# Kernel optimization log

Hardware: AMD Instinct MI355X
Metric: run time of the kernel (lower is better)

The kernel has to match this reference:

```python
import jax, jax.numpy as jnp
import numpy as np

LN_EPS = 1e-5

def setup_inputs() -> dict:
    key = jax.random.key(0)
    k1, k2, k3 = jax.random.split(key, 3)
    B, S, D = 4, 4096, 768
    seq_feat = jax.random.normal(k1, (B, S, D), dtype=jnp.float32)
    msa_feat = jax.random.normal(k2, (B, S, D), dtype=jnp.float32)
    ln_gamma = jnp.ones((2 * D,), dtype=jnp.float32)
    ln_beta = jnp.zeros((2 * D,), dtype=jnp.float32)
    # torch init zeroes gate weight; use small random weights for a non-degenerate test
    gate_w = jax.random.normal(k3, (2, 2 * D), dtype=jnp.float32) * 0.02
    gate_b = jnp.zeros((2,), dtype=jnp.float32)
    return {"seq_feat": seq_feat, "msa_feat": msa_feat, "ln_gamma": ln_gamma,
            "ln_beta": ln_beta, "gate_w": gate_w, "gate_b": gate_b}

def reference(seq_feat, msa_feat, ln_gamma, ln_beta, gate_w, gate_b):
    # h: [B, S, 2D]
    h = jnp.concatenate([seq_feat, msa_feat], axis=-1)
    mean = jnp.mean(h, axis=-1, keepdims=True)
    var = jnp.mean(jnp.square(h - mean), axis=-1, keepdims=True)
    hn = (h - mean) * jax.lax.rsqrt(var + LN_EPS) * ln_gamma + ln_beta
    # dropout in eval mode = identity
    logits = jnp.einsum('bsd,kd->bsk', hn, gate_w) + gate_b  # [B, S, 2]
    w = jax.nn.softmax(logits, axis=-1)
    return w[..., 0:1] * seq_feat + w[..., 1:2] * msa_feat
```

## Files before the change

### kernel.cpp

```cpp
#include <hip/hip_runtime.h>

#define LN_EPS 1e-5f
#define D 768
#define TWO_D 1536

__global__ __launch_bounds__(256) void fused_gate_kernel(
    const float* __restrict__ seq, const float* __restrict__ msa,
    const float* __restrict__ gamma, const float* __restrict__ beta,
    const float* __restrict__ gate_w, const float* __restrict__ gate_b,
    float* __restrict__ out, int nrows)
{
    const int wave = threadIdx.x >> 6;
    const int lane = threadIdx.x & 63;
    const int row = blockIdx.x * 4 + wave;
    if (row >= nrows) return;

    const float4* seq4 = (const float4*)(seq + (size_t)row * D);
    const float4* msa4 = (const float4*)(msa + (size_t)row * D);

    float4 s[3], m[3];
    #pragma unroll
    for (int j = 0; j < 3; ++j) {
        s[j] = seq4[j * 64 + lane];
        m[j] = msa4[j * 64 + lane];
    }

    float sum = 0.f, sumsq = 0.f;
    #pragma unroll
    for (int j = 0; j < 3; ++j) {
        sum   += s[j].x + s[j].y + s[j].z + s[j].w
               + m[j].x + m[j].y + m[j].z + m[j].w;
        sumsq += s[j].x*s[j].x + s[j].y*s[j].y + s[j].z*s[j].z + s[j].w*s[j].w
               + m[j].x*m[j].x + m[j].y*m[j].y + m[j].z*m[j].z + m[j].w*m[j].w;
    }
    #pragma unroll
    for (int off = 32; off > 0; off >>= 1) {
        sum   += __shfl_xor(sum,   off, 64);
        sumsq += __shfl_xor(sumsq, off, 64);
    }
    const float inv_n = 1.f / (float)TWO_D;
    const float mean = sum * inv_n;
    const float var  = fmaxf(sumsq * inv_n - mean * mean, 0.f);
    const float rstd = rsqrtf(var + LN_EPS);

    const float4* g4  = (const float4*)gamma;
    const float4* b4  = (const float4*)beta;
    const float4* w04 = (const float4*)gate_w;
    const float4* w14 = (const float4*)(gate_w + TWO_D);
    float l0 = 0.f, l1 = 0.f;
    #pragma unroll
    for (int j = 0; j < 3; ++j) {
        const int i4s = j * 64 + lane;
        {
            float4 g = g4[i4s], bb = b4[i4s], w0 = w04[i4s], w1 = w14[i4s];
            float hx = (s[j].x - mean) * rstd * g.x + bb.x;
            float hy = (s[j].y - mean) * rstd * g.y + bb.y;
            float hz = (s[j].z - mean) * rstd * g.z + bb.z;
            float hw = (s[j].w - mean) * rstd * g.w + bb.w;
            l0 += hx * w0.x + hy * w0.y + hz * w0.z + hw * w0.w;
            l1 += hx * w1.x + hy * w1.y + hz * w1.z + hw * w1.w;
        }
        const int i4m = (D / 4) + i4s;
        {
            float4 g = g4[i4m], bb = b4[i4m], w0 = w04[i4m], w1 = w14[i4m];
            float hx = (m[j].x - mean) * rstd * g.x + bb.x;
            float hy = (m[j].y - mean) * rstd * g.y + bb.y;
            float hz = (m[j].z - mean) * rstd * g.z + bb.z;
            float hw = (m[j].w - mean) * rstd * g.w + bb.w;
            l0 += hx * w0.x + hy * w0.y + hz * w0.z + hw * w0.w;
            l1 += hx * w1.x + hy * w1.y + hz * w1.z + hw * w1.w;
        }
    }
    #pragma unroll
    for (int off = 32; off > 0; off >>= 1) {
        l0 += __shfl_xor(l0, off, 64);
        l1 += __shfl_xor(l1, off, 64);
    }
    l0 += gate_b[0];
    l1 += gate_b[1];

    const float mx = fmaxf(l0, l1);
    const float e0 = __expf(l0 - mx);
    const float e1 = __expf(l1 - mx);
    const float inv = 1.f / (e0 + e1);
    const float w0s = e0 * inv;
    const float w1s = e1 * inv;

    float4* out4 = (float4*)(out + (size_t)row * D);
    #pragma unroll
    for (int j = 0; j < 3; ++j) {
        float4 o;
        o.x = w0s * s[j].x + w1s * m[j].x;
        o.y = w0s * s[j].y + w1s * m[j].y;
        o.z = w0s * s[j].z + w1s * m[j].z;
        o.w = w0s * s[j].w + w1s * m[j].w;
        out4[j * 64 + lane] = o;
    }
}

extern "C" void kernel_launch(void* const* d_in, const int* in_sizes, int n_in,
                              void* d_out, int out_size, void* d_ws, size_t ws_size,
                              hipStream_t stream) {
    const float* seq    = (const float*)d_in[0];
    const float* msa    = (const float*)d_in[1];
    const float* gamma  = (const float*)d_in[2];
    const float* beta   = (const float*)d_in[3];
    const float* gate_w = (const float*)d_in[4];
    const float* gate_b = (const float*)d_in[5];
    float* out = (float*)d_out;

    const int nrows = in_sizes[0] / D;
    const int blocks = (nrows + 3) / 4;
    fused_gate_kernel<<<blocks, 256, 0, stream>>>(
        seq, msa, gamma, beta, gate_w, gate_b, out, nrows);
}
```

Baseline: 148.9 us.

## Fold LayerNorm affine into gate weights and process two rows per persistent wave

Precomputes gamma*w products and beta·w constants once per wave, so each row's logit becomes rstd*(x·P - mean*C) + E and needs no per-element normalisation. The grid becomes persistent (1024 blocks, grid-stride) and each wave handles two rows per iteration to get more loads in flight. Register pressure rises from holding 12 float4 row registers plus 12 float4 folded weights, and launch_bounds asks for 4 blocks per SM. The kernel is memory bound, so the saved ALU work may matter less than the extra memory-level parallelism.

Result: slower. 188.1 us (+26.3%).

```diff
diff --git a/kernel.cpp b/kernel.cpp
--- a/kernel.cpp
+++ b/kernel.cpp
@@ -2,99 +2,153 @@
 
 #define LN_EPS 1e-5f
 #define D 768
+#define D4 192
 #define TWO_D 1536
 
-__global__ __launch_bounds__(256) void fused_gate_kernel(
+__global__ __launch_bounds__(256, 4) void fused_gate_kernel(
     const float* __restrict__ seq, const float* __restrict__ msa,
     const float* __restrict__ gamma, const float* __restrict__ beta,
     const float* __restrict__ gate_w, const float* __restrict__ gate_b,
-    float* __restrict__ out, int nrows)
+    float* __restrict__ out, int nrows, int nwaves)
 {
-    const int wave = threadIdx.x >> 6;
     const int lane = threadIdx.x & 63;
-    const int row = blockIdx.x * 4 + wave;
-    if (row >= nrows) return;
-
-    const float4* seq4 = (const float4*)(seq + (size_t)row * D);
-    const float4* msa4 = (const float4*)(msa + (size_t)row * D);
-
-    float4 s[3], m[3];
-    #pragma unroll
-    for (int j = 0; j < 3; ++j) {
-        s[j] = seq4[j * 64 + lane];
-        m[j] = msa4[j * 64 + lane];
-    }
-
-    float sum = 0.f, sumsq = 0.f;
-    #pragma unroll
-    for (int j = 0; j < 3; ++j) {
-        sum   += s[j].x + s[j].y + s[j].z + s[j].w
-               + m[j].x + m[j].y + m[j].z + m[j].w;
-        sumsq += s[j].x*s[j].x + s[j].y*s[j].y + s[j].z*s[j].z + s[j].w*s[j].w
-               + m[j].x*m[j].x + m[j].y*m[j].y + m[j].z*m[j].z + m[j].w*m[j].w;
-    }
-    #pragma unroll
-    for (int off = 32; off > 0; off >>= 1) {
-        sum   += __shfl_xor(sum,   off, 64);
-        sumsq += __shfl_xor(sumsq, off, 64);
-    }
-    const float inv_n = 1.f / (float)TWO_D;
-    const float mean = sum * inv_n;
-    const float var  = fmaxf(sumsq * inv_n - mean * mean, 0.f);
-    const float rstd = rsqrtf(var + LN_EPS);
+    const int wid  = (int)((blockIdx.x * blockDim.x + threadIdx.x) >> 6);
 
     const float4* g4  = (const float4*)gamma;
     const float4* b4  = (const float4*)beta;
     const float4* w04 = (const float4*)gate_w;
     const float4* w14 = (const float4*)(gate_w + TWO_D);
-    float l0 = 0.f, l1 = 0.f;
+
+    float4 P0[6], P1[6];
+    float C0 = 0.f, C1 = 0.f, E0 = 0.f, E1 = 0.f;
     #pragma unroll
-    for (int j = 0; j < 3; ++j) {
-        const int i4s = j * 64 + lane;
-        {
-            float4 g = g4[i4s], bb = b4[i4s], w0 = w04[i4s], w1 = w14[i4s];
-            float hx = (s[j].x - mean) * rstd * g.x + bb.x;
-            float hy = (s[j].y - mean) * rstd * g.y + bb.y;
-            float hz = (s[j].z - mean) * rstd * g.z + bb.z;
-            float hw = (s[j].w - mean) * rstd * g.w + bb.w;
-            l0 += hx * w0.x + hy * w0.y + hz * w0.z + hw * w0.w;
-            l1 += hx * w1.x + hy * w1.y + hz * w1.z + hw * w1.w;
-        }
-        const int i4m = (D / 4) + i4s;
-        {
-            float4 g = g4[i4m], bb = b4[i4m], w0 = w04[i4m], w1 = w14[i4m];
-            float hx = (m[j].x - mean) * rstd * g.x + bb.x;
-            float hy = (m[j].y - mean) * rstd * g.y + bb.y;
-            float hz = (m[j].z - mean) * rstd * g.z + bb.z;
-            float hw = (m[j].w - mean) * rstd * g.w + bb.w;
-            l0 += hx * w0.x + hy * w0.y + hz * w0.z + hw * w0.w;
-            l1 += hx * w1.x + hy * w1.y + hz * w1.z + hw * w1.w;
-        }
+    for (int j = 0; j < 6; ++j) {
+        const int idx = (j < 3) ? (j * 64 + lane) : (D4 + (j - 3) * 64 + lane);
+        float4 g = g4[idx], bb = b4[idx], w0 = w04[idx], w1 = w14[idx];
+        P0[j].x = g.x * w0.x; P0[j].y = g.y * w0.y; P0[j].z = g.z * w0.z; P0[j].w = g.w * w0.w;
+        P1[j].x = g.x * w1.x; P1[j].y = g.y * w1.y; P1[j].z = g.z * w1.z; P1[j].w = g.w * w1.w;
+        C0 += P0[j].x + P0[j].y + P0[j].z + P0[j].w;
+        C1 += P1[j].x + P1[j].y + P1[j].z + P1[j].w;
+        E0 += bb.x * w0.x + bb.y * w0.y + bb.z * w0.z + bb.w * w0.w;
+        E1 += bb.x * w1.x + bb.y * w1.y + bb.z * w1.z + bb.w * w1.w;
     }
     #pragma unroll
     for (int off = 32; off > 0; off >>= 1) {
-        l0 += __shfl_xor(l0, off, 64);
-        l1 += __shfl_xor(l1, off, 64);
+        C0 += __shfl_xor(C0, off, 64);
+        C1 += __shfl_xor(C1, off, 64);
+        E0 += __shfl_xor(E0, off, 64);
+        E1 += __shfl_xor(E1, off, 64);
     }
-    l0 += gate_b[0];
-    l1 += gate_b[1];
+    const float gb0 = gate_b[0], gb1 = gate_b[1];
+    const float inv_n = 1.f / (float)TWO_D;
 
-    const float mx = fmaxf(l0, l1);
-    const float e0 = __expf(l0 - mx);
-    const float e1 = __expf(l1 - mx);
-    const float inv = 1.f / (e0 + e1);
-    const float w0s = e0 * inv;
-    const float w1s = e1 * inv;
+    for (int base = wid * 2; base < nrows; base += nwaves * 2) {
+        const int r0 = base;
+        const bool has1 = (base + 1) < nrows;
+        const int r1 = has1 ? (base + 1) : base;
 
-    float4* out4 = (float4*)(out + (size_t)row * D);
-    #pragma unroll
-    for (int j = 0; j < 3; ++j) {
-        float4 o;
-        o.x = w0s * s[j].x + w1s * m[j].x;
-        o.y = w0s * s[j].y + w1s * m[j].y;
-        o.z = w0s * s[j].z + w1s * m[j].z;
-        o.w = w0s * s[j].w + w1s * m[j].w;
-        out4[j * 64 + lane] = o;
+        const float4* s0p = (const float4*)(seq + (size_t)r0 * D);
+        const float4* m0p = (const float4*)(msa + (size_t)r0 * D);
+        const float4* s1p = (const float4*)(seq + (size_t)r1 * D);
+        const float4* m1p = (const float4*)(msa + (size_t)r1 * D);
+
+        float4 s0[3], m0[3], s1[3], m1[3];
+        #pragma unroll
+        for (int j = 0; j < 3; ++j) {
+            s0[j] = s0p[j * 64 + lane];
+            m0[j] = m0p[j * 64 + lane];
+            s1[j] = s1p[j * 64 + lane];
+            m1[j] = m1p[j * 64 + lane];
+        }
+
+        float su0 = 0.f, sq0 = 0.f, a00 = 0.f, a01 = 0.f;
+        float su1 = 0.f, sq1 = 0.f, a10 = 0.f, a11 = 0.f;
+        #pragma unroll
+        for (int j = 0; j < 3; ++j) {
+            {
+                float4 h = s0[j];
+                su0 += h.x + h.y + h.z + h.w;
+                sq0 += h.x*h.x + h.y*h.y + h.z*h.z + h.w*h.w;
+                a00 += h.x*P0[j].x + h.y*P0[j].y + h.z*P0[j].z + h.w*P0[j].w;
+                a01 += h.x*P1[j].x + h.y*P1[j].y + h.z*P1[j].z + h.w*P1[j].w;
+            }
+            {
+                float4 h = m0[j];
+                su0 += h.x + h.y + h.z + h.w;
+                sq0 += h.x*h.x + h.y*h.y + h.z*h.z + h.w*h.w;
+                a00 += h.x*P0[j+3].x + h.y*P0[j+3].y + h.z*P0[j+3].z + h.w*P0[j+3].w;
+                a01 += h.x*P1[j+3].x + h.y*P1[j+3].y + h.z*P1[j+3].z + h.w*P1[j+3].w;
+            }
+            {
+                float4 h = s1[j];
+                su1 += h.x + h.y + h.z + h.w;
+                sq1 += h.x*h.x + h.y*h.y + h.z*h.z + h.w*h.w;
+                a10 += h.x*P0[j].x + h.y*P0[j].y + h.z*P0[j].z + h.w*P0[j].w;
+                a11 += h.x*P1[j].x + h.y*P1[j].y + h.z*P1[j].z + h.w*P1[j].w;
+            }
+            {
+                float4 h = m1[j];
+                su1 += h.x + h.y + h.z + h.w;
+                sq1 += h.x*h.x + h.y*h.y + h.z*h.z + h.w*h.w;
+                a10 += h.x*P0[j+3].x + h.y*P0[j+3].y + h.z*P0[j+3].z + h.w*P0[j+3].w;
+                a11 += h.x*P1[j+3].x + h.y*P1[j+3].y + h.z*P1[j+3].z + h.w*P1[j+3].w;
+            }
+        }
+
+        #pragma unroll
+        for (int off = 32; off > 0; off >>= 1) {
+            su0 += __shfl_xor(su0, off, 64);
+            sq0 += __shfl_xor(sq0, off, 64);
+            a00 += __shfl_xor(a00, off, 64);
+            a01 += __shfl_xor(a01, off, 64);
+            su1 += __shfl_xor(su1, off, 64);
+            sq1 += __shfl_xor(sq1, off, 64);
+            a10 += __shfl_xor(a10, off, 64);
+            a11 += __shfl_xor(a11, off, 64);
+        }
+
+        {
+            const float mean = su0 * inv_n;
+            const float var  = fmaxf(sq0 * inv_n - mean * mean, 0.f);
+            const float rstd = rsqrtf(var + LN_EPS);
+            const float l0 = rstd * (a00 - mean * C0) + E0 + gb0;
+            const float l1 = rstd * (a01 - mean * C1) + E1 + gb1;
+            const float mx = fmaxf(l0, l1);
+            const float e0 = __expf(l0 - mx), e1 = __expf(l1 - mx);
+            const float inv = 1.f / (e0 + e1);
+            const float w0s = e0 * inv, w1s = e1 * inv;
+            float4* o4 = (float4*)(out + (size_t)r0 * D);
+            #pragma unroll
+            for (int j = 0; j < 3; ++j) {
+                float4 o;
+                o.x = w0s * s0[j].x + w1s * m0[j].x;
+                o.y = w0s * s0[j].y + w1s * m0[j].y;
+                o.z = w0s * s0[j].z + w1s * m0[j].z;
+                o.w = w0s * s0[j].w + w1s * m0[j].w;
+                o4[j * 64 + lane] = o;
+            }
+        }
+        if (has1) {
+            const float mean = su1 * inv_n;
+            const float var  = fmaxf(sq1 * inv_n - mean * mean, 0.f);
+            const float rstd = rsqrtf(var + LN_EPS);
+            const float l0 = rstd * (a10 - mean * C0) + E0 + gb0;
+            const float l1 = rstd * (a11 - mean * C1) + E1 + gb1;
+            const float mx = fmaxf(l0, l1);
+            const float e0 = __expf(l0 - mx), e1 = __expf(l1 - mx);
+            const float inv = 1.f / (e0 + e1);
+            const float w0s = e0 * inv, w1s = e1 * inv;
+            float4* o4 = (float4*)(out + (size_t)r1 * D);
+            #pragma unroll
+            for (int j = 0; j < 3; ++j) {
+                float4 o;
+                o.x = w0s * s1[j].x + w1s * m1[j].x;
+                o.y = w0s * s1[j].y + w1s * m1[j].y;
+                o.z = w0s * s1[j].z + w1s * m1[j].z;
+                o.w = w0s * s1[j].w + w1s * m1[j].w;
+                o4[j * 64 + lane] = o;
+            }
+        }
     }
 }
 
@@ -110,7 +164,8 @@
     float* out = (float*)d_out;
 
     const int nrows = in_sizes[0] / D;
-    const int blocks = (nrows + 3) / 4;
+    const int blocks = 1024;
+    const int nwaves = blocks * 4;
     fused_gate_kernel<<<blocks, 256, 0, stream>>>(
-        seq, msa, gamma, beta, gate_w, gate_b, out, nrows);
+        seq, msa, gamma, beta, gate_w, gate_b, out, nrows, nwaves);
 }
```

## Fold LayerNorm affine into gate weights via setup kernel, single-pass reduction

Applied to the files above, without the earlier changes.

Adds a tiny setup kernel that precomputes gamma*w products and constant terms (sum of gamma*w, beta·w plus bias) into the workspace. The main kernel then computes sum, sum of squares and the two raw dot products in one pass with a single combined shuffle reduction, and derives the logits algebraically. This removes the second reduction round and the gamma/beta loads per row, at the cost of an extra kernel launch and workspace traffic.

New measurement: 146.4 us. About the same (-1.7%).

```diff
diff --git a/kernel.cpp b/kernel.cpp
--- a/kernel.cpp
+++ b/kernel.cpp
@@ -2,91 +2,108 @@
 
 #define LN_EPS 1e-5f
 #define D 768
+#define D4 192
 #define TWO_D 1536
+
+
+__global__ __launch_bounds__(64) void setup_kernel(
+    const float* __restrict__ gamma, const float* __restrict__ beta,
+    const float* __restrict__ gate_w, const float* __restrict__ gate_b,
+    float* __restrict__ ws)
+{
+    const int lane = threadIdx.x;
+    const float4* g4  = (const float4*)gamma;
+    const float4* b4  = (const float4*)beta;
+    const float4* w04 = (const float4*)gate_w;
+    const float4* w14 = (const float4*)(gate_w + TWO_D);
+    float4* P04 = (float4*)ws;
+    float4* P14 = (float4*)(ws + TWO_D);
+
+    float C0 = 0.f, C1 = 0.f, E0 = 0.f, E1 = 0.f;
+    #pragma unroll
+    for (int j = 0; j < 6; ++j) {
+        const int idx = j * 64 + lane;
+        float4 g = g4[idx], bb = b4[idx], w0 = w04[idx], w1 = w14[idx];
+        float4 p0, p1;
+        p0.x = g.x * w0.x; p0.y = g.y * w0.y; p0.z = g.z * w0.z; p0.w = g.w * w0.w;
+        p1.x = g.x * w1.x; p1.y = g.y * w1.y; p1.z = g.z * w1.z; p1.w = g.w * w1.w;
+        P04[idx] = p0;
+        P14[idx] = p1;
+        C0 += p0.x + p0.y + p0.z + p0.w;
+        C1 += p1.x + p1.y + p1.z + p1.w;
+        E0 += bb.x * w0.x + bb.y * w0.y + bb.z * w0.z + bb.w * w0.w;
+        E1 += bb.x * w1.x + bb.y * w1.y + bb.z * w1.z + bb.w * w1.w;
+    }
+    #pragma unroll
+    for (int off = 32; off > 0; off >>= 1) {
+        C0 += __shfl_xor(C0, off, 64);
+        C1 += __shfl_xor(C1, off, 64);
+        E0 += __shfl_xor(E0, off, 64);
+        E1 += __shfl_xor(E1, off, 64);
+    }
+    if (lane == 0) {
+        float* c = ws + 2 * TWO_D;
+        c[0] = C0;
+        c[1] = C1;
+        c[2] = E0 + gate_b[0];
+        c[3] = E1 + gate_b[1];
+    }
+}
 
 __global__ __launch_bounds__(256) void fused_gate_kernel(
     const float* __restrict__ seq, const float* __restrict__ msa,
-    const float* __restrict__ gamma, const float* __restrict__ beta,
-    const float* __restrict__ gate_w, const float* __restrict__ gate_b,
-    float* __restrict__ out, int nrows)
+    const float* __restrict__ ws, float* __restrict__ out, int nrows)
 {
     const int wave = threadIdx.x >> 6;
     const int lane = threadIdx.x & 63;
     const int row = blockIdx.x * 4 + wave;
     if (row >= nrows) return;
 
-    const float4* seq4 = (const float4*)(seq + (size_t)row * D);
-    const float4* msa4 = (const float4*)(msa + (size_t)row * D);
+    const float4* s4 = (const float4*)(seq + (size_t)row * D);
+    const float4* m4 = (const float4*)(msa + (size_t)row * D);
+    const float4* P04 = (const float4*)ws;
+    const float4* P14 = (const float4*)(ws + TWO_D);
 
     float4 s[3], m[3];
     #pragma unroll
     for (int j = 0; j < 3; ++j) {
-        s[j] = seq4[j * 64 + lane];
-        m[j] = msa4[j * 64 + lane];
+        s[j] = s4[j * 64 + lane];
+        m[j] = m4[j * 64 + lane];
     }
+    const float4 cst = *(const float4*)(ws + 2 * TWO_D);
 
-    float sum = 0.f, sumsq = 0.f;
+    float su = 0.f, sq = 0.f, a0 = 0.f, a1 = 0.f;
     #pragma unroll
-    for (int j = 0; j < 3; ++j) {
-        sum   += s[j].x + s[j].y + s[j].z + s[j].w
-               + m[j].x + m[j].y + m[j].z + m[j].w;
-        sumsq += s[j].x*s[j].x + s[j].y*s[j].y + s[j].z*s[j].z + s[j].w*s[j].w
-               + m[j].x*m[j].x + m[j].y*m[j].y + m[j].z*m[j].z + m[j].w*m[j].w;
+    for (int j = 0; j < 6; ++j) {
+        const int idx = (j < 3) ? (j * 64 + lane) : (D4 + (j - 3) * 64 + lane);
+        const float4 p0 = P04[idx];
+        const float4 p1 = P14[idx];
+        const float4 h = (j < 3) ? s[j] : m[j - 3];
+        su += h.x + h.y + h.z + h.w;
+        sq += h.x * h.x + h.y * h.y + h.z * h.z + h.w * h.w;
+        a0 += h.x * p0.x + h.y * p0.y + h.z * p0.z + h.w * p0.w;
+        a1 += h.x * p1.x + h.y * p1.y + h.z * p1.z + h.w * p1.w;
     }
     #pragma unroll
     for (int off = 32; off > 0; off >>= 1) {
-        sum   += __shfl_xor(sum,   off, 64);
-        sumsq += __shfl_xor(sumsq, off, 64);
+        su += __shfl_xor(su, off, 64);
+        sq += __shfl_xor(sq, off, 64);
+        a0 += __shfl_xor(a0, off, 64);
+        a1 += __shfl_xor(a1, off, 64);
     }
+
     const float inv_n = 1.f / (float)TWO_D;
-    const float mean = sum * inv_n;
-    const float var  = fmaxf(sumsq * inv_n - mean * mean, 0.f);
+    const float mean = su * inv_n;
+    const float var  = fmaxf(sq * inv_n - mean * mean, 0.f);
     const float rstd = rsqrtf(var + LN_EPS);
+    const float l0 = rstd * (a0 - mean * cst.x) + cst.z;
+    const float l1 = rstd * (a1 - mean * cst.y) + cst.w;
+    const float mx = fmaxf(l0, l1);
+    const float e0 = __expf(l0 - mx), e1 = __expf(l1 - mx);
+    const float inv = 1.f / (e0 + e1);
+    const float w0s = e0 * inv, w1s = e1 * inv;
 
-    const float4* g4  = (const float4*)gamma;
-    const float4* b4  = (const float4*)beta;
-    const float4* w04 = (const float4*)gate_w;
-    const float4* w14 = (const float4*)(gate_w + TWO_D);
-    float l0 = 0.f, l1 = 0.f;
-    #pragma unroll
-    for (int j = 0; j < 3; ++j) {
-        const int i4s = j * 64 + lane;
-        {
-            float4 g = g4[i4s], bb = b4[i4s], w0 = w04[i4s], w1 = w14[i4s];
-            float hx = (s[j].x - mean) * rstd * g.x + bb.x;
-            float hy = (s[j].y - mean) * rstd * g.y + bb.y;
-            float hz = (s[j].z - mean) * rstd * g.z + bb.z;
-            float hw = (s[j].w - mean) * rstd * g.w + bb.w;
-            l0 += hx * w0.x + hy * w0.y + hz * w0.z + hw * w0.w;
-            l1 += hx * w1.x + hy * w1.y + hz * w1.z + hw * w1.w;
-        }
-        const int i4m = (D / 4) + i4s;
-        {
-            float4 g = g4[i4m], bb = b4[i4m], w0 = w04[i4m], w1 = w14[i4m];
-            float hx = (m[j].x - mean) * rstd * g.x + bb.x;
-            float hy = (m[j].y - mean) * rstd * g.y + bb.y;
-            float hz = (m[j].z - mean) * rstd * g.z + bb.z;
-            float hw = (m[j].w - mean) * rstd * g.w + bb.w;
-            l0 += hx * w0.x + hy * w0.y + hz * w0.z + hw * w0.w;
-            l1 += hx * w1.x + hy * w1.y + hz * w1.z + hw * w1.w;
-        }
-    }
-    #pragma unroll
-    for (int off = 32; off > 0; off >>= 1) {
-        l0 += __shfl_xor(l0, off, 64);
-        l1 += __shfl_xor(l1, off, 64);
-    }
-    l0 += gate_b[0];
-    l1 += gate_b[1];
-
-    const float mx = fmaxf(l0, l1);
-    const float e0 = __expf(l0 - mx);
-    const float e1 = __expf(l1 - mx);
-    const float inv = 1.f / (e0 + e1);
-    const float w0s = e0 * inv;
-    const float w1s = e1 * inv;
-
-    float4* out4 = (float4*)(out + (size_t)row * D);
+    float4* o4 = (float4*)(out + (size_t)row * D);
     #pragma unroll
     for (int j = 0; j < 3; ++j) {
         float4 o;
@@ -94,7 +111,7 @@
         o.y = w0s * s[j].y + w1s * m[j].y;
         o.z = w0s * s[j].z + w1s * m[j].z;
         o.w = w0s * s[j].w + w1s * m[j].w;
-        out4[j * 64 + lane] = o;
+        o4[j * 64 + lane] = o;
     }
 }
 
@@ -108,9 +125,9 @@
     const float* gate_w = (const float*)d_in[4];
     const float* gate_b = (const float*)d_in[5];
     float* out = (float*)d_out;
+    float* ws  = (float*)d_ws;
 
     const int nrows = in_sizes[0] / D;
-    const int blocks = (nrows + 3) / 4;
-    fused_gate_kernel<<<blocks, 256, 0, stream>>>(
-        seq, msa, gamma, beta, gate_w, gate_b, out, nrows);
+    setup_kernel<<<1, 64, 0, stream>>>(gamma, beta, gate_w, gate_b, ws);
+    fused_gate_kernel<<<(nrows + 3) / 4, 256, 0, stream>>>(seq, msa, ws, out, nrows);
 }
```
